# Optimization experiments

Measured on AMD Instinct MI355X. Metric: run time of the kernel, lower is better.

The kernel has to match this reference:

```python
import jax, jax.numpy as jnp
from jax import lax
import numpy as np

K = 32          # PyG radius_graph default max_num_neighbors
NEG = -1e9      # mask fill for max-aggregation


def _gather(a, i):  # a [N,C], i [...,] int -> a[i]
    return a[i]


def radius_knn(pos, r):
    # pos [B,N,3] -> (idx [B,N,K], valid [B,N,K]) nearest-K within radius r, self excluded
    sq = jnp.sum(pos * pos, -1)                                   # [B,N]
    d2 = sq[:, :, None] + sq[:, None, :] - 2.0 * jnp.einsum('bnc,bmc->bnm', pos, pos)
    N = pos.shape[1]
    d2 = d2 + jnp.eye(N, dtype=pos.dtype) * 1e9                    # exclude self-loops
    neg, idx = lax.top_k(-d2, K)
    valid = (-neg) <= r * r
    return idx, valid


def fps(pos, n):
    # iterative farthest point sampling, deterministic start at index 0; pos [B,N,3] -> idx [B,n]
    def one(p):
        mind0 = jnp.sum((p - p[0]) ** 2, -1)
        def step(mind, _):
            i = jnp.argmax(mind)
            nd = jnp.sum((p - p[i]) ** 2, -1)
            return jnp.minimum(mind, nd), i
        _, idxs = lax.scan(step, mind0, None, length=n - 1)
        return jnp.concatenate([jnp.zeros((1,), jnp.int32), idxs.astype(jnp.int32)])
    return jax.vmap(one)(pos)


def point_conv(x, pos, idx, valid, W1, b1, W2, b2):
    # PyG PointNetConv: msg = local_nn(concat(x_j, pos_j - pos_i)), max-aggregate
    g = jax.vmap(_gather)
    rel = g(pos, idx) - pos[:, :, None, :]                         # [B,N,K,3]
    feat = rel if x is None else jnp.concatenate([g(x, idx), rel], -1)
    h = jax.nn.relu(feat @ W1 + b1) @ W2 + b2                      # [B,N,K,C]
    h = jnp.where(valid[..., None], h, NEG)
    return jnp.max(h, axis=2)                                      # [B,N,C]


def _forward(pos, W1a, b1a, W1b, b1b, W2a, b2a, W2b, b2b, W3a, b3a, W3b, b3b,
             Wc1, bc1, Wc2, bc2, Wc3, bc3, Wd1, bd1, Wd2, bd2):
    take = jax.vmap(_gather)
    B, N, _ = pos.shape
    idx, v = radius_knn(pos, 0.2)
    x = jax.nn.relu(point_conv(None, pos, idx, v, W1a, b1a, W1b, b1b))
    fi = fps(pos, N // 2)
    x, pos = take(x, fi), take(pos, fi)
    idx, v = radius_knn(pos, 0.4)
    x = jax.nn.relu(point_conv(x, pos, idx, v, W2a, b2a, W2b, b2b))
    fi = fps(pos, N // 8)
    x, pos = take(x, fi), take(pos, fi)
    idx, v = radius_knn(pos, 1.0)
    x = jax.nn.relu(point_conv(x, pos, idx, v, W3a, b3a, W3b, b3b))
    feat = jnp.max(x, axis=1)                                      # global max pool [B,256]
    h = jax.nn.relu(feat @ Wc1 + bc1)
    h = jax.nn.relu(h @ Wc2 + bc2)                                 # dropout is identity in eval
    logits = h @ Wc3 + bc3
    h2 = jax.nn.relu(feat @ Wd1 + bd1)
    d = h2 @ Wd2 + bd2
    return jax.nn.log_softmax(logits, axis=-1), jax.nn.log_softmax(d, axis=-1)


def setup_inputs() -> dict:
    key = jax.random.key(0)
    ks = jax.random.split(key, 32)
    def lin(k, fin, fout):
        kw, kb = jax.random.split(k)
        s = 1.0 / np.sqrt(fin)
        return (jax.random.uniform(kw, (fin, fout), jnp.float32, -s, s),
                jax.random.uniform(kb, (fout,), jnp.float32, -s, s))
    inp = {'pos': jax.random.uniform(ks[0], (8, 4096, 3), jnp.float32)}
    names = [('W1a','b1a',3,64),('W1b','b1b',64,64),('W2a','b2a',67,128),('W2b','b2b',128,128),
             ('W3a','b3a',131,256),('W3b','b3b',256,256),('Wc1','bc1',256,256),('Wc2','bc2',256,256),
             ('Wc3','bc3',256,40),('Wd1','bd1',256,256),('Wd2','bd2',256,2)]
    for i, (wn, bn, fin, fout) in enumerate(names):
        W, b = lin(ks[i + 1], fin, fout)
        inp[wn], inp[bn] = W, b
    return inp


def reference(pos, W1a, b1a, W1b, b1b, W2a, b2a, W2b, b2b, W3a, b3a, W3b, b3b,
              Wc1, bc1, Wc2, bc2, Wc3, bc3, Wd1, bd1, Wd2, bd2):
    return _forward(pos, W1a, b1a, W1b, b1b, W2a, b2a, W2b, b2b, W3a, b3a, W3b, b3b,
                    Wc1, bc1, Wc2, bc2, Wc3, bc3, Wd1, bd1, Wd2, bd2)
```

## Files before the change

### kernel.cpp

```cpp
#include <hip/hip_runtime.h>


#define NB 8

__device__ __forceinline__ unsigned obits(float f) {
  unsigned u = __float_as_uint(f);
  return (u & 0x80000000u) ? ~u : (u | 0x80000000u);
}

static constexpr int CAND = 1024;

template<int CTRL>
__device__ __forceinline__ unsigned long long dpp_max_step(unsigned long long v) {
  const int lo = (int)(unsigned)(v & 0xffffffffull);
  const int hi = (int)(unsigned)(v >> 32);
  const unsigned nlo = (unsigned)__builtin_amdgcn_update_dpp(lo, lo, CTRL, 0xf, 0xf, false);
  const unsigned nhi = (unsigned)__builtin_amdgcn_update_dpp(hi, hi, CTRL, 0xf, 0xf, false);
  const unsigned long long nv = ((unsigned long long)nhi << 32) | nlo;
  return (nv > v) ? nv : v;
}

__device__ __forceinline__ unsigned wave_iscan_add(unsigned x) {
  x += (unsigned)__builtin_amdgcn_update_dpp(0, (int)x, 0x111, 0xf, 0xf, true);
  x += (unsigned)__builtin_amdgcn_update_dpp(0, (int)x, 0x112, 0xf, 0xf, true);
  x += (unsigned)__builtin_amdgcn_update_dpp(0, (int)x, 0x114, 0xf, 0xf, true);
  x += (unsigned)__builtin_amdgcn_update_dpp(0, (int)x, 0x118, 0xf, 0xf, true);
  x += (unsigned)__builtin_amdgcn_update_dpp(0, (int)x, 0x142, 0xa, 0xf, true);
  x += (unsigned)__builtin_amdgcn_update_dpp(0, (int)x, 0x143, 0xc, 0xf, true);
  return x;
}

__device__ __forceinline__ unsigned long long u64max(unsigned long long a,
                                                    unsigned long long b) {
  return (b > a) ? b : a;
}

__device__ __forceinline__ void set_wave_prio_hi() {
#if __has_builtin(__builtin_amdgcn_s_setprio)
  __builtin_amdgcn_s_setprio(3);
#endif
}

template<int N, int NOUT, int T>
__device__ __forceinline__ void fps_body(char* sm, const float* __restrict__ pb,
                                         int* __restrict__ fi, int b) {
  constexpr int P = N / T;
  constexpr int NW = T / 64;
  int4* sPosI = (int4*)sm;
  int*  sfi   = (int*)(sm + (size_t)N * 16);
  unsigned long long* sKey =
      (unsigned long long*)(sm + (size_t)N * 16 + NOUT * 4);
  const int tid = threadIdx.x, wid = tid >> 6, lane = tid & 63;
  set_wave_prio_hi();
  int ix[P], iy[P], iz[P];
  unsigned long long mind[P];
  for (int t = tid; t < N; t += T) {
    sPosI[t] = make_int4((int)(pb[3*t]   * 8388608.f),
                         (int)(pb[3*t+1] * 8388608.f),
                         (int)(pb[3*t+2] * 8388608.f), 0);
  }
  __syncthreads();
  const int x0 = sPosI[0].x, y0 = sPosI[0].y, z0 = sPosI[0].z;
  const int invBase = 4095 - tid * P;
  unsigned long long bv;
  {
    unsigned long long tv[P];
#pragma unroll
    for (int e = 0; e < P; e++) {
      const int j = tid * P + e;
      const int4 p4 = sPosI[j];
      ix[e] = p4.x; iy[e] = p4.y; iz[e] = p4.z;
      const long long dx = p4.x - x0, dy = p4.y - y0, dz = p4.z - z0;
      const unsigned long long d2 =
          (unsigned long long)(dx * dx + dy * dy + dz * dz);
      const unsigned long long k = (d2 << 12) | (unsigned)(invBase - e);
      mind[e] = k; tv[e] = k;
    }
#pragma unroll
    for (int s = 1; s < P; s <<= 1)
#pragma unroll
      for (int e = 0; e + s < P; e += 2 * s)
        if (tv[e + s] > tv[e]) tv[e] = tv[e + s];
    bv = tv[0];
  }
  if (tid == 0) sfi[0] = 0;
  for (int t = 1; t < NOUT; t++) {
    unsigned long long v = bv;
    v = dpp_max_step<0x111>(v);
    v = dpp_max_step<0x112>(v);
    v = dpp_max_step<0x114>(v);
    v = dpp_max_step<0x118>(v);
    v = dpp_max_step<0x142>(v);
    v = dpp_max_step<0x143>(v);
    const int pp = t & 1;
    if (lane == 63) sKey[pp * NW + wid] = v;
    __syncthreads();
    unsigned long long best;
    if (NW == 8) {
      unsigned long long k0 = sKey[pp*8+0], k1 = sKey[pp*8+1],
                         k2 = sKey[pp*8+2], k3 = sKey[pp*8+3],
                         k4 = sKey[pp*8+4], k5 = sKey[pp*8+5],
                         k6 = sKey[pp*8+6], k7 = sKey[pp*8+7];
      k0 = u64max(k0, k1); k2 = u64max(k2, k3);
      k4 = u64max(k4, k5); k6 = u64max(k6, k7);
      k0 = u64max(k0, k2); k4 = u64max(k4, k6);
      best = u64max(k0, k4);
    } else {
      unsigned long long k0 = sKey[pp*NW+0];
#pragma unroll
      for (int w2 = 1; w2 < NW; w2++) k0 = u64max(k0, sKey[pp*NW+w2]);
      best = k0;
    }
    const int ii = 4095 - (int)(best & 0xFFFull);
    if (tid == 0) sfi[t] = ii;
    const int4 wc = sPosI[ii];
    unsigned long long tv[P];
#pragma unroll
    for (int e = 0; e < P; e++) {
      const long long dx = ix[e] - wc.x, dy = iy[e] - wc.y, dz = iz[e] - wc.z;
      const unsigned long long nd =
          (unsigned long long)(dx * dx + dy * dy + dz * dz);
      const unsigned long long nk = (nd << 12) | (unsigned)(invBase - e);
      unsigned long long mk = mind[e];
      mk = (nk < mk) ? nk : mk;
      mind[e] = mk;
      tv[e] = mk;
    }
#pragma unroll
    for (int s = 1; s < P; s <<= 1)
#pragma unroll
      for (int e = 0; e + s < P; e += 2 * s)
        if (tv[e + s] > tv[e]) tv[e] = tv[e + s];
    bv = tv[0];
  }
  __syncthreads();
  for (int t = tid; t < NOUT; t += T) fi[(size_t)b * NOUT + t] = sfi[t];
}

template<int N, int H, int C, bool HASX, bool FOLDMAX, int T>
__device__ __forceinline__ void knnconv_body(
    char* sm, const float* __restrict__ pb, int b, int i,
    const float* __restrict__ U, const float* __restrict__ Wrel,
    const float* __restrict__ b1, const float* __restrict__ W2,
    const float* __restrict__ b2, float* __restrict__ out, double rr) {
  constexpr int HCHUNK = (C == 64) ? 64 : (C == 128 ? 32 : 16);
  constexpr int STR = HCHUNK + 4;
  constexpr int NW = T / 64;
  constexpr int EPK = 32 / NW;
  constexpr int BPT = 2048 / T;
  constexpr int KNNFRONT = N * 8 + 13312;
  constexpr int CONVFRONT = 32 * H * 4 + C * STR * 4 + NW * C * 4;
  constexpr int FRONT = (KNNFRONT > CONVFRONT) ? KNNFRONT : CONVFRONT;
  double*   d2s     = (double*)sm;
  unsigned* hist    = (unsigned*)(sm + N * 8);
  int*      candIdx = (int*)(sm + N * 8 + 8192);
  unsigned* sWT     = (unsigned*)(sm + N * 8 + 12288);
  float* h1s  = (float*)sm;
  float* sW2T = (float*)(sm + 32 * H * 4);
  float* sRed = (float*)(sm + 32 * H * 4 + C * STR * 4);
  int*   snbr = (int*)(sm + FRONT);
  float* rel  = (float*)(sm + FRONT + 128);
  int*   pcnt = (int*)(sm + FRONT + 128 + 384);
  int*   pbin = pcnt + 1;
  const int tid = threadIdx.x;

  const double xi = pb[3*i], yi = pb[3*i+1], zi = pb[3*i+2];
  const double si = (xi*xi + yi*yi) + zi*zi;
  for (int t = tid; t < 2048; t += T) hist[t] = 0u;
  if (tid == 0) *pcnt = 0;
  __syncthreads();
  for (int j = tid; j < N; j += T) {
    double xj = pb[3*j], yj = pb[3*j+1], zj = pb[3*j+2];
    double sj = (xj*xj + yj*yj) + zj*zj;
    double dt = (xi*xj + yi*yj) + zi*zj;
    double d2 = (si + sj) - 2.0*dt;
    if (j == i) d2 += 1e9;
    d2s[j] = d2;
    atomicAdd(&hist[obits((float)d2) >> 21], 1u);
  }
  __syncthreads();
  unsigned lsum = 0;
  const int base = tid * BPT;
#pragma unroll
  for (int q = 0; q < BPT; q++) lsum += hist[base + q];
  const unsigned isc = wave_iscan_add(lsum);
  if ((tid & 63) == 63) sWT[tid >> 6] = isc;
  __syncthreads();
  {
    const int wid = tid >> 6;
    unsigned offs = 0;
#pragma unroll
    for (int w2 = 0; w2 < NW; w2++) offs += (w2 < wid) ? sWT[w2] : 0u;
    const unsigned incl = isc + offs, excl = incl - lsum;
    if (excl < 32u && incl >= 32u) {
      unsigned c = excl;
      for (int q = 0; q < BPT; q++) {
        c += hist[base + q];
        if (c >= 32u) { *pbin = base + q; break; }
      }
    }
  }
  __syncthreads();
  const int binT = *pbin;
  for (int j = tid; j < N; j += T) {
    if ((int)(obits((float)d2s[j]) >> 21) <= binT) {
      int p = atomicAdd(pcnt, 1);
      if (p < CAND) candIdx[p] = j;
    }
  }
  __syncthreads();
  const int M = min(*pcnt, CAND);
  for (int c = tid; c < M; c += T) {
    const int j = candIdx[c];
    const double d = d2s[j];
    int rank = 0;
    for (int e = 0; e < M; e++) {
      const int j2 = candIdx[e];
      const double de = d2s[j2];
      rank += (de < d || (de == d && j2 < j)) ? 1 : 0;
    }
    if (rank < 32) snbr[rank] = (d <= rr) ? j : -1;
  }
  __syncthreads();

  if (tid < 32) {
    const int j = snbr[tid];
    float rx = 0.f, ry = 0.f, rz = 0.f;
    if (j >= 0) {
      rx = pb[3*j]   - pb[3*i];
      ry = pb[3*j+1] - pb[3*i+1];
      rz = pb[3*j+2] - pb[3*i+2];
    }
    rel[tid*3+0] = rx; rel[tid*3+1] = ry; rel[tid*3+2] = rz;
  }
  __syncthreads();

  constexpr int QPK = H / 4;
  for (int qi = tid; qi < 32 * QPK; qi += T) {
    const int k = qi / QPK, h0 = (qi - k * QPK) * 4;
    const int j = snbr[k];
    float4 v = make_float4(0.f, 0.f, 0.f, 0.f);
    if (j >= 0) {
      float4 a = HASX ? *(const float4*)&U[((size_t)b * N + j) * H + h0]
                      : *(const float4*)&b1[h0];
      const float rx = rel[k*3], ry = rel[k*3+1], rz = rel[k*3+2];
      const float4 w0 = *(const float4*)&Wrel[h0];
      const float4 w1 = *(const float4*)&Wrel[H + h0];
      const float4 w2 = *(const float4*)&Wrel[2 * H + h0];
      a.x += rx * w0.x + ry * w1.x + rz * w2.x;
      a.y += rx * w0.y + ry * w1.y + rz * w2.y;
      a.z += rx * w0.z + ry * w1.z + rz * w2.z;
      a.w += rx * w0.w + ry * w1.w + rz * w2.w;
      v = make_float4(fmaxf(a.x, 0.f), fmaxf(a.y, 0.f),
                      fmaxf(a.z, 0.f), fmaxf(a.w, 0.f));
    }
    *(float4*)&h1s[k * H + h0] = v;
  }
  const int cc = tid & 63;
  const int kk = tid >> 6;
  constexpr int CC = C / 64;
  float acc[EPK][CC];
#pragma unroll
  for (int e = 0; e < EPK; e++)
#pragma unroll
    for (int q = 0; q < CC; q++) acc[e][q] = 0.f;
  for (int hc = 0; hc < H; hc += HCHUNK) {
    __syncthreads();
    for (int idx = tid; idx < HCHUNK * C; idx += T) {
      const int hh = idx / C, c = idx - hh * C;
      sW2T[c * STR + hh] = W2[(size_t)(hc + hh) * C + c];
    }
    __syncthreads();
    for (int hh0 = 0; hh0 < HCHUNK; hh0 += 4) {
      float4 wv[CC];
#pragma unroll
      for (int q = 0; q < CC; q++)
        wv[q] = *(const float4*)&sW2T[(cc + q * 64) * STR + hh0];
#pragma unroll
      for (int e = 0; e < EPK; e++) {
        const float4 hv = *(const float4*)&h1s[(kk + e * NW) * H + hc + hh0];
#pragma unroll
        for (int q = 0; q < CC; q++) {
          acc[e][q] += hv.x * wv[q].x;
          acc[e][q] += hv.y * wv[q].y;
          acc[e][q] += hv.z * wv[q].z;
          acc[e][q] += hv.w * wv[q].w;
        }
      }
    }
  }
  float m[CC];
#pragma unroll
  for (int q = 0; q < CC; q++) m[q] = -1e9f;
#pragma unroll
  for (int e = 0; e < EPK; e++) {
    if (snbr[kk + e * NW] >= 0) {
#pragma unroll
      for (int q = 0; q < CC; q++) m[q] = fmaxf(m[q], acc[e][q]);
    }
  }
#pragma unroll
  for (int q = 0; q < CC; q++) sRed[kk * C + cc + q * 64] = m[q];
  __syncthreads();
  if (kk == 0) {
#pragma unroll
    for (int q = 0; q < CC; q++) {
      const int c = cc + q * 64;
      float mm = sRed[c];
#pragma unroll
      for (int w2 = 1; w2 < NW; w2++) mm = fmaxf(mm, sRed[w2 * C + c]);
      const float o = (mm > -5e8f) ? (mm + b2[c]) : -1e9f;
      const float r = fmaxf(o, 0.f);
      if (FOLDMAX) {
        atomicMax((int*)&out[b * C + c], __float_as_int(r));
      } else {
        out[((size_t)b * N + i) * C + c] = r;
      }
    }
  }
}

template<int N, int NOUT, int H, int C, bool HASX, int SMSIZE>
__device__ __forceinline__ void stage_fused_impl(
    const float* pos, double rr, int* fi, const float* U, const float* Wrel,
    const float* b1, const float* W2, const float* b2, float* out, char* sm) {
  if (blockIdx.x < NB) {
    fps_body<N, NOUT, 512>(sm, pos + (size_t)blockIdx.x * N * 3, fi, blockIdx.x);
  } else {
    const int row = blockIdx.x - NB;
    const int b = row / N;
    const int i = row - b * N;
    knnconv_body<N, H, C, HASX, false, 512>(sm, pos + (size_t)b * N * 3, b, i,
                                            U, Wrel, b1, W2, b2, out, rr);
  }
}

__global__ __attribute__((amdgpu_waves_per_eu(2, 2))) __launch_bounds__(512, 2)
void stage1_kernel(const float* __restrict__ pos, double rr, int* __restrict__ fi,
                   const float* __restrict__ Wrel, const float* __restrict__ b1,
                   const float* __restrict__ W2, const float* __restrict__ b2,
                   float* __restrict__ out) {
  __shared__ __align__(16) char sm[82944];
  stage_fused_impl<4096, 2048, 64, 64, false, 82944>(
      pos, rr, fi, nullptr, Wrel, b1, W2, b2, out, sm);
}

__global__ __attribute__((amdgpu_waves_per_eu(2, 2))) __launch_bounds__(512, 2)
void stage2_kernel(const float* __restrict__ pos, double rr, int* __restrict__ fi,
                   const float* __restrict__ U, const float* __restrict__ Wrel,
                   const float* __restrict__ b1, const float* __restrict__ W2,
                   const float* __restrict__ b2, float* __restrict__ out) {
  __shared__ __align__(16) char sm[39440];
  stage_fused_impl<2048, 512, 128, 128, true, 39440>(
      pos, rr, fi, U, Wrel, b1, W2, b2, out, sm);
}

__global__ __launch_bounds__(512)
void stage3_kernel(const float* __restrict__ pos, double rr,
                   const float* __restrict__ U, const float* __restrict__ Wrel,
                   const float* __restrict__ b1, const float* __restrict__ W2,
                   const float* __restrict__ b2, float* __restrict__ feat) {
  __shared__ __align__(16) char sm[61968];
  const int b = blockIdx.x / 512;
  const int i = blockIdx.x - b * 512;
  knnconv_body<512, 256, 256, true, true, 512>(sm, pos + (size_t)b * 512 * 3,
                                               b, i, U, Wrel, b1, W2, b2,
                                               feat, rr);
}

template<int CIN, int HH>
__global__ __launch_bounds__(HH)
void gp_kernel(const float* __restrict__ X, const float* __restrict__ posPrev,
               const int* __restrict__ fi, int Nprev, int M,
               const float* __restrict__ W, const float* __restrict__ bias,
               float* __restrict__ U, float* __restrict__ posDst) {
  const int row = blockIdx.x;
  const int b = row / M;
  const int tid = threadIdx.x;
  const int j = fi[row];
  __shared__ float sx[CIN];
  if (tid < CIN) sx[tid] = X[((size_t)b * Nprev + j) * CIN + tid];
  if (tid < 3) posDst[(size_t)row * 3 + tid] = posPrev[((size_t)b * Nprev + j) * 3 + tid];
  __syncthreads();
  float a = bias[tid];
  for (int f = 0; f < CIN; f++) a = fmaf(sx[f], W[f * HH + tid], a);
  U[(size_t)row * HH + tid] = a;
}

__global__ __launch_bounds__(256) void head_kernel(
    const float* __restrict__ feat,
    const float* __restrict__ Wc1, const float* __restrict__ bc1,
    const float* __restrict__ Wc2, const float* __restrict__ bc2,
    const float* __restrict__ Wc3, const float* __restrict__ bc3,
    const float* __restrict__ Wd1, const float* __restrict__ bd1,
    const float* __restrict__ Wd2, const float* __restrict__ bd2,
    float* __restrict__ out) {
  const int b = blockIdx.x, tid = threadIdx.x;
  __shared__ float sf[256], sh[256], sh2[256], shd[256], sl[48];
  sf[tid] = feat[b * 256 + tid];
  __syncthreads();
  float a = bc1[tid], ad = bd1[tid];
  for (int f = 0; f < 256; f++) {
    const float fv = sf[f];
    a  = fmaf(fv, Wc1[f * 256 + tid], a);
    ad = fmaf(fv, Wd1[f * 256 + tid], ad);
  }
  sh[tid] = fmaxf(a, 0.f);
  shd[tid] = fmaxf(ad, 0.f);
  __syncthreads();
  float a2 = bc2[tid];
  for (int f = 0; f < 256; f++) a2 = fmaf(sh[f], Wc2[f * 256 + tid], a2);
  sh2[tid] = fmaxf(a2, 0.f);
  __syncthreads();
  if (tid < 40) {
    float l = bc3[tid];
    for (int f = 0; f < 256; f++) l = fmaf(sh2[f], Wc3[f * 40 + tid], l);
    sl[tid] = l;
  }
  if (tid >= 64 && tid < 66) {
    const int q = tid - 64;
    float l = bd2[q];
    for (int f = 0; f < 256; f++) l = fmaf(shd[f], Wd2[f * 2 + q], l);
    sl[40 + q] = l;
  }
  __syncthreads();
  if (tid == 0) {
    float m0 = sl[0];
    for (int q = 1; q < 40; q++) m0 = fmaxf(m0, sl[q]);
    float s = 0.f;
    for (int q = 0; q < 40; q++) s += expf(sl[q] - m0);
    const float ls = logf(s);
    for (int q = 0; q < 40; q++) out[b * 40 + q] = sl[q] - m0 - ls;
    const float m1 = fmaxf(sl[40], sl[41]);
    const float s1 = expf(sl[40] - m1) + expf(sl[41] - m1);
    const float ls1 = logf(s1);
    out[320 + b * 2 + 0] = sl[40] - m1 - ls1;
    out[320 + b * 2 + 1] = sl[41] - m1 - ls1;
  }
}

extern "C" void kernel_launch(void* const* d_in, const int* in_sizes, int n_in,
                              void* d_out, int out_size, void* d_ws, size_t ws_size,
                              hipStream_t stream) {
  (void)in_sizes; (void)n_in; (void)out_size; (void)ws_size;
  const float* pos = (const float*)d_in[0];
  const float* W1a = (const float*)d_in[1];  const float* b1a = (const float*)d_in[2];
  const float* W1b = (const float*)d_in[3];  const float* b1b = (const float*)d_in[4];
  const float* W2a = (const float*)d_in[5];  const float* b2a = (const float*)d_in[6];
  const float* W2b = (const float*)d_in[7];  const float* b2b = (const float*)d_in[8];
  const float* W3a = (const float*)d_in[9];  const float* b3a = (const float*)d_in[10];
  const float* W3b = (const float*)d_in[11]; const float* b3b = (const float*)d_in[12];
  const float* Wc1 = (const float*)d_in[13]; const float* bc1 = (const float*)d_in[14];
  const float* Wc2 = (const float*)d_in[15]; const float* bc2 = (const float*)d_in[16];
  const float* Wc3 = (const float*)d_in[17]; const float* bc3 = (const float*)d_in[18];
  const float* Wd1 = (const float*)d_in[19]; const float* bd1 = (const float*)d_in[20];
  const float* Wd2 = (const float*)d_in[21]; const float* bd2 = (const float*)d_in[22];
  float* out = (float*)d_out;

  char* w = (char*)d_ws;
  auto alloc = [&](size_t bytes) -> void* {
    void* p = (void*)w;
    w += (bytes + 255) & ~(size_t)255;
    return p;
  };
  int*   fi1  = (int*)  alloc((size_t)NB*2048*4);
  float* x1   = (float*)alloc((size_t)NB*4096*64*4);
  float* pos2 = (float*)alloc((size_t)NB*2048*3*4);
  float* U2   = (float*)alloc((size_t)NB*2048*128*4);
  float* x2   = (float*)alloc((size_t)NB*2048*128*4);
  int*   fi2  = (int*)  alloc((size_t)NB*512*4);
  float* pos3 = (float*)alloc((size_t)NB*512*3*4);
  float* U3   = (float*)alloc((size_t)NB*512*256*4);
  float* feat = (float*)alloc((size_t)NB*256*4);

  hipMemsetAsync(feat, 0, (size_t)NB * 256 * 4, stream);

  stage1_kernel<<<NB + NB * 4096, 512, 0, stream>>>(
      pos, 0.2 * 0.2, fi1, W1a, b1a, W1b, b1b, x1);

  gp_kernel<64, 128><<<NB * 2048, 128, 0, stream>>>(
      x1, pos, fi1, 4096, 2048, W2a, b2a, U2, pos2);

  stage2_kernel<<<NB + NB * 2048, 512, 0, stream>>>(
      pos2, 0.4 * 0.4, fi2, U2, W2a + (size_t)64 * 128, b2a, W2b, b2b, x2);

  gp_kernel<128, 256><<<NB * 512, 256, 0, stream>>>(
      x2, pos2, fi2, 2048, 512, W3a, b3a, U3, pos3);

  stage3_kernel<<<NB * 512, 512, 0, stream>>>(
      pos3, 1.0, U3, W3a + (size_t)128 * 256, b3a, W3b, b3b, feat);

  head_kernel<<<NB, 256, 0, stream>>>(feat, Wc1, bc1, Wc2, bc2, Wc3, bc3,
                                      Wd1, bd1, Wd2, bd2, out);
}
```

Measured before the change: 2.900 ms.

## Select two FPS points per iteration via top-2 reduction when provably equivalent

The farthest point sampling loop now reduces the top-2 min-distance keys across the block instead of only the maximum. If the runner-up point stays at least as far from the first pick as its current min distance, it is provably the next FPS choice, so both points are emitted in one iteration and the distance update uses both centers. This aims to halve the number of serial block-wide barriers and reductions in the latency-bound FPS loop. The cost is a more expensive top-2 DPP/shared reduction and extra per-element work on every iteration.

```diff
diff --git a/kernel.cpp b/kernel.cpp
--- a/kernel.cpp
+++ b/kernel.cpp
@@ -11,13 +11,12 @@
 static constexpr int CAND = 1024;
 
 template<int CTRL>
-__device__ __forceinline__ unsigned long long dpp_max_step(unsigned long long v) {
+__device__ __forceinline__ unsigned long long dpp_mov0_u64(unsigned long long v) {
   const int lo = (int)(unsigned)(v & 0xffffffffull);
   const int hi = (int)(unsigned)(v >> 32);
-  const unsigned nlo = (unsigned)__builtin_amdgcn_update_dpp(lo, lo, CTRL, 0xf, 0xf, false);
-  const unsigned nhi = (unsigned)__builtin_amdgcn_update_dpp(hi, hi, CTRL, 0xf, 0xf, false);
-  const unsigned long long nv = ((unsigned long long)nhi << 32) | nlo;
-  return (nv > v) ? nv : v;
+  const unsigned nlo = (unsigned)__builtin_amdgcn_update_dpp(0, lo, CTRL, 0xf, 0xf, true);
+  const unsigned nhi = (unsigned)__builtin_amdgcn_update_dpp(0, hi, CTRL, 0xf, 0xf, true);
+  return ((unsigned long long)nhi << 32) | nlo;
 }
 
 __device__ __forceinline__ unsigned wave_iscan_add(unsigned x) {
@@ -34,6 +33,10 @@
                                                     unsigned long long b) {
   return (b > a) ? b : a;
 }
+__device__ __forceinline__ unsigned long long u64min(unsigned long long a,
+                                                    unsigned long long b) {
+  return (b < a) ? b : a;
+}
 
 __device__ __forceinline__ void set_wave_prio_hi() {
 #if __has_builtin(__builtin_amdgcn_s_setprio)
@@ -48,8 +51,8 @@
   constexpr int NW = T / 64;
   int4* sPosI = (int4*)sm;
   int*  sfi   = (int*)(sm + (size_t)N * 16);
-  unsigned long long* sKey =
-      (unsigned long long*)(sm + (size_t)N * 16 + NOUT * 4);
+  ulonglong2* sKey =
+      (ulonglong2*)(sm + (size_t)N * 16 + NOUT * 4);
   const int tid = threadIdx.x, wid = tid >> 6, lane = tid & 63;
   set_wave_prio_hi();
   int ix[P], iy[P], iz[P];
@@ -62,7 +65,7 @@
   __syncthreads();
   const int x0 = sPosI[0].x, y0 = sPosI[0].y, z0 = sPosI[0].z;
   const int invBase = 4095 - tid * P;
-  unsigned long long bv;
+  unsigned long long bv1, bv2;
   {
     unsigned long long tv[P];
 #pragma unroll
@@ -80,61 +83,102 @@
     for (int s = 1; s < P; s <<= 1)
 #pragma unroll
       for (int e = 0; e + s < P; e += 2 * s)
-        if (tv[e + s] > tv[e]) tv[e] = tv[e + s];
-    bv = tv[0];
+        tv[e] = u64max(tv[e], tv[e + s]);
+    bv1 = tv[0];
+    unsigned long long s2 = 0ull;
+#pragma unroll
+    for (int e = 0; e < P; e++)
+      s2 = u64max(s2, (mind[e] == bv1) ? 0ull : mind[e]);
+    bv2 = s2;
   }
   if (tid == 0) sfi[0] = 0;
-  for (int t = 1; t < NOUT; t++) {
-    unsigned long long v = bv;
-    v = dpp_max_step<0x111>(v);
-    v = dpp_max_step<0x112>(v);
-    v = dpp_max_step<0x114>(v);
-    v = dpp_max_step<0x118>(v);
-    v = dpp_max_step<0x142>(v);
-    v = dpp_max_step<0x143>(v);
-    const int pp = t & 1;
-    if (lane == 63) sKey[pp * NW + wid] = v;
+  int t = 1, pp = 0;
+  while (t < NOUT) {
+    unsigned long long a1 = bv1, a2 = bv2;
+#define TOP2_STEP(CTRL)                                                   \
+    {                                                                     \
+      const unsigned long long o1 = dpp_mov0_u64<CTRL>(a1);               \
+      const unsigned long long o2 = dpp_mov0_u64<CTRL>(a2);               \
+      const unsigned long long n1 = u64max(a1, o1);                       \
+      const unsigned long long n2 = u64max(u64min(a1, o1), u64max(a2, o2)); \
+      a1 = n1; a2 = n2;                                                   \
+    }
+    TOP2_STEP(0x111)
+    TOP2_STEP(0x112)
+    TOP2_STEP(0x114)
+    TOP2_STEP(0x118)
+    TOP2_STEP(0x142)
+    TOP2_STEP(0x143)
+#undef TOP2_STEP
+    if (lane == 63) sKey[pp * NW + wid] = make_ulonglong2(a1, a2);
     __syncthreads();
-    unsigned long long best;
-    if (NW == 8) {
-      unsigned long long k0 = sKey[pp*8+0], k1 = sKey[pp*8+1],
-                         k2 = sKey[pp*8+2], k3 = sKey[pp*8+3],
-                         k4 = sKey[pp*8+4], k5 = sKey[pp*8+5],
-                         k6 = sKey[pp*8+6], k7 = sKey[pp*8+7];
-      k0 = u64max(k0, k1); k2 = u64max(k2, k3);
-      k4 = u64max(k4, k5); k6 = u64max(k6, k7);
-      k0 = u64max(k0, k2); k4 = u64max(k4, k6);
-      best = u64max(k0, k4);
+    ulonglong2 kv[NW];
+#pragma unroll
+    for (int w2 = 0; w2 < NW; w2++) kv[w2] = sKey[pp * NW + w2];
+#pragma unroll
+    for (int s = 1; s < NW; s <<= 1)
+#pragma unroll
+      for (int w2 = 0; w2 + s < NW; w2 += 2 * s) {
+        const unsigned long long n1 = u64max(kv[w2].x, kv[w2 + s].x);
+        const unsigned long long n2 =
+            u64max(u64min(kv[w2].x, kv[w2 + s].x), u64max(kv[w2].y, kv[w2 + s].y));
+        kv[w2] = make_ulonglong2(n1, n2);
+      }
+    const unsigned long long K1 = kv[0].x, K2 = kv[0].y;
+    const int w1 = 4095 - (int)(K1 & 0xFFFull);
+    const int4 c1 = sPosI[w1];
+    const int r  = 4095 - (int)(K2 & 0xFFFull);
+    const int4 c2 = sPosI[r];
+    const long long rdx = c2.x - c1.x, rdy = c2.y - c1.y, rdz = c2.z - c1.z;
+    const unsigned long long d2rw =
+        (unsigned long long)(rdx * rdx + rdy * rdy + rdz * rdz);
+    const bool paired = (t + 1 < NOUT) && (d2rw >= (K2 >> 12));
+    if (tid == 0) {
+      sfi[t] = w1;
+      if (paired) sfi[t + 1] = r;
+    }
+    unsigned long long tv[P];
+    if (paired) {
+#pragma unroll
+      for (int e = 0; e < P; e++) {
+        const long long dx = ix[e] - c1.x, dy = iy[e] - c1.y, dz = iz[e] - c1.z;
+        const long long ex = ix[e] - c2.x, ey = iy[e] - c2.y, ez = iz[e] - c2.z;
+        const unsigned long long nd1 =
+            (unsigned long long)(dx * dx + dy * dy + dz * dz);
+        const unsigned long long nd2 =
+            (unsigned long long)(ex * ex + ey * ey + ez * ez);
+        const unsigned long long nd = u64min(nd1, nd2);
+        const unsigned long long nk = (nd << 12) | (unsigned)(invBase - e);
+        const unsigned long long mk = u64min(mind[e], nk);
+        mind[e] = mk; tv[e] = mk;
+      }
     } else {
-      unsigned long long k0 = sKey[pp*NW+0];
-#pragma unroll
-      for (int w2 = 1; w2 < NW; w2++) k0 = u64max(k0, sKey[pp*NW+w2]);
-      best = k0;
-    }
-    const int ii = 4095 - (int)(best & 0xFFFull);
-    if (tid == 0) sfi[t] = ii;
-    const int4 wc = sPosI[ii];
-    unsigned long long tv[P];
-#pragma unroll
-    for (int e = 0; e < P; e++) {
-      const long long dx = ix[e] - wc.x, dy = iy[e] - wc.y, dz = iz[e] - wc.z;
-      const unsigned long long nd =
-          (unsigned long long)(dx * dx + dy * dy + dz * dz);
-      const unsigned long long nk = (nd << 12) | (unsigned)(invBase - e);
-      unsigned long long mk = mind[e];
-      mk = (nk < mk) ? nk : mk;
-      mind[e] = mk;
-      tv[e] = mk;
+#pragma unroll
+      for (int e = 0; e < P; e++) {
+        const long long dx = ix[e] - c1.x, dy = iy[e] - c1.y, dz = iz[e] - c1.z;
+        const unsigned long long nd =
+            (unsigned long long)(dx * dx + dy * dy + dz * dz);
+        const unsigned long long nk = (nd << 12) | (unsigned)(invBase - e);
+        const unsigned long long mk = u64min(mind[e], nk);
+        mind[e] = mk; tv[e] = mk;
+      }
     }
 #pragma unroll
     for (int s = 1; s < P; s <<= 1)
 #pragma unroll
       for (int e = 0; e + s < P; e += 2 * s)
-        if (tv[e + s] > tv[e]) tv[e] = tv[e + s];
-    bv = tv[0];
-  }
-  __syncthreads();
-  for (int t = tid; t < NOUT; t += T) fi[(size_t)b * NOUT + t] = sfi[t];
+        tv[e] = u64max(tv[e], tv[e + s]);
+    bv1 = tv[0];
+    unsigned long long s2 = 0ull;
+#pragma unroll
+    for (int e = 0; e < P; e++)
+      s2 = u64max(s2, (mind[e] == bv1) ? 0ull : mind[e]);
+    bv2 = s2;
+    t += paired ? 2 : 1;
+    pp ^= 1;
+  }
+  __syncthreads();
+  for (int t2 = tid; t2 < NOUT; t2 += T) fi[(size_t)b * NOUT + t2] = sfi[t2];
 }
 
 template<int N, int H, int C, bool HASX, bool FOLDMAX, int T>
```

New measurement: 3.744 ms. 1.29x slower.
